# Kernel optimization log

Hardware: AMD Instinct MI355X
Metric: run time of the kernel (lower is better)

The kernel has to match this reference:

```python
import jax, jax.numpy as jnp
import numpy as np

NI = 256        # in_channels
QK = NI // 8    # query/key channels = 32
BS, H, W = 4, 64, 64


def setup_inputs() -> dict:
    key = jax.random.key(0)
    ks = jax.random.split(key, 8)
    x = jax.random.normal(ks[0], (BS, NI, H, W), dtype=jnp.float32)
    # 1x1 conv weights stored as [out_ch, in_ch] (kernel is 1x1)
    wq = jax.random.normal(ks[1], (QK, NI), dtype=jnp.float32) * (1.0 / np.sqrt(NI))
    bq = jnp.zeros((QK,), dtype=jnp.float32)
    wk = jax.random.normal(ks[2], (QK, NI), dtype=jnp.float32) * (1.0 / np.sqrt(NI))
    bk = jnp.zeros((QK,), dtype=jnp.float32)
    wv = jax.random.normal(ks[3], (NI, NI), dtype=jnp.float32) * (1.0 / np.sqrt(NI))
    bv = jnp.zeros((NI,), dtype=jnp.float32)
    # gamma is zero-init in the module; use small random values so the
    # attention branch actually contributes (post-training state).
    gamma = jax.random.normal(ks[4], (1, NI, 1, 1), dtype=jnp.float32) * 0.1
    return {"x": x, "wq": wq, "bq": bq, "wk": wk, "bk": bk,
            "wv": wv, "bv": bv, "gamma": gamma}


def reference(x, wq, bq, wk, bk, wv, bv, gamma):
    bs, c, h, w = x.shape
    n = h * w
    xf = x.reshape(bs, c, n)                       # [bs, c, N]
    # 1x1 convs == per-pixel linear maps over channels
    q = jnp.einsum('oc,bcn->bno', wq, xf) + bq     # [bs, N, qk]
    k = jnp.einsum('oc,bcn->bon', wk, xf) + bk[None, :, None]  # [bs, qk, N]
    v = jnp.einsum('oc,bcn->bon', wv, xf) + bv[None, :, None]  # [bs, c, N]
    attn = jax.nn.softmax(jnp.einsum('bnq,bqm->bnm', q, k), axis=-1)  # [bs, N, N]
    out = jnp.einsum('bcm,bnm->bcn', v, attn)      # value @ attn^T
    out = out.reshape(bs, c, h, w)
    return gamma * out + x
```

## Files before the change

kernel.cpp:

```cpp
#include <hip/hip_runtime.h>
#include <cstdint>
#include <cstddef>

#define NI   256
#define QKC  32
#define BS   4
#define NPIX 4096
#define LOG2E 1.4426950408889634f

typedef __bf16 bf16x8 __attribute__((ext_vector_type(8)));
typedef __bf16 bf16x4 __attribute__((ext_vector_type(4)));
typedef float  f32x16 __attribute__((ext_vector_type(16)));

__device__ inline f32x16 zero16() {
    f32x16 z;
    #pragma unroll
    for (int i = 0; i < 16; ++i) z[i] = 0.f;
    return z;
}

__global__ __launch_bounds__(256) void wconv_pack(
    const float* __restrict__ wq, const float* __restrict__ wk,
    const float* __restrict__ wv, __bf16* __restrict__ wpk)
{
    int f = blockIdx.x * 256 + threadIdx.x;
    int otl = f >> 10, rem = f & 1023;
    int kk = rem >> 6, h = (rem >> 5) & 1, l31 = rem & 31;
    int och = otl * 32 + l31, c0 = kk * 16 + 8 * h;
    const float* src = och < 32 ? wq + och * NI + c0
                     : och < 64 ? wk + (och - 32) * NI + c0
                                : wv + (och - 64) * NI + c0;
    float4 x0 = *(const float4*)src;
    float4 x1 = *(const float4*)(src + 4);
    __align__(16) __bf16 o8[8] = {
        (__bf16)x0.x, (__bf16)x0.y, (__bf16)x0.z, (__bf16)x0.w,
        (__bf16)x1.x, (__bf16)x1.y, (__bf16)x1.z, (__bf16)x1.w};
    *(uint4*)(wpk + (size_t)f * 8) = *(const uint4*)o8;
}

__global__ __launch_bounds__(256) void qkv_mfma(
    const float* __restrict__ x, const __bf16* __restrict__ wpk,
    const float* __restrict__ bq, const float* __restrict__ bk,
    const float* __restrict__ bv,
    __bf16* __restrict__ qpk, __bf16* __restrict__ kpk, __bf16* __restrict__ vpk)
{
    __shared__ __align__(16) __bf16 xT[32][264];
    __shared__ float bls[320];

    const int t = threadIdx.x, w = t >> 6, lane = t & 63;
    const int l31 = lane & 31, h = lane >> 5;
    const int b = blockIdx.y, n0 = blockIdx.x * 32, kt = blockIdx.x;

    for (int i = t; i < 320; i += 256)
        bls[i] = i < 32 ? bq[i] : i < 64 ? bk[i - 32] : bv[i - 64];

    {
        int n4 = (t & 7) * 4, cb = (t >> 3) * 8;
        float4 xv[8];
        #pragma unroll
        for (int j = 0; j < 8; ++j)
            xv[j] = *(const float4*)(x + ((size_t)(b * NI) + cb + j) * NPIX + n0 + n4);
        #pragma unroll
        for (int i = 0; i < 4; ++i) {
            __align__(16) __bf16 r8[8];
            #pragma unroll
            for (int j = 0; j < 8; ++j) r8[j] = (__bf16)((&xv[j].x)[i]);
            *(uint4*)&xT[n4 + i][cb] = *(const uint4*)r8;
        }
    }
    __syncthreads();

    f32x16 acc[3] = {zero16(), zero16(), zero16()};
    #pragma unroll 4
    for (int kk = 0; kk < 16; ++kk) {
        bf16x8 xf = *(const bf16x8*)&xT[l31][kk * 16 + 8 * h];
        #pragma unroll
        for (int jj = 0; jj < 3; ++jj) {
            int otl = w + 4 * jj;
            if (otl < 10) {
                bf16x8 wf = *(const bf16x8*)(wpk + (size_t)((otl * 16 + kk) * 64 + 32 * h + l31) * 8);
                acc[jj] = __builtin_amdgcn_mfma_f32_32x32x16_bf16(wf, xf, acc[jj], 0, 0, 0);
            }
        }
    }
    __syncthreads();

    __bf16 (*vT)[264] = xT;
    #pragma unroll
    for (int jj = 0; jj < 3; ++jj) {
        int otl = w + 4 * jj;
        if (otl >= 2 && otl < 10) {
            #pragma unroll
            for (int qd = 0; qd < 4; ++qd) {
                int c0v = (otl - 2) * 32 + 8 * qd + 4 * h;
                __align__(8) __bf16 q4[4];
                #pragma unroll
                for (int i = 0; i < 4; ++i)
                    q4[i] = (__bf16)(acc[jj][4 * qd + i] + bls[64 + c0v + i]);
                *(uint2*)&vT[l31][c0v] = *(const uint2*)q4;
            }
        }
    }
    #pragma unroll
    for (int jj = 0; jj < 3; ++jj) {
        int otl = w + 4 * jj;
        if (otl == 0) {
            #pragma unroll
            for (int kc = 0; kc < 2; ++kc) {
                __align__(16) __bf16 hi8[8];
                #pragma unroll
                for (int j = 0; j < 8; ++j) {
                    int r = 8 * kc + j;
                    int och = (r & 3) + 8 * (r >> 2) + 4 * h;
                    hi8[j] = (__bf16)((acc[jj][r] + bls[och]) * LOG2E);
                }
                size_t base = ((((size_t)(b * 128 + kt) * 2 + 0) * 2 + kc) * 2 + h) * 32 + l31;
                *(uint4*)(qpk + base * 8) = *(const uint4*)hi8;
            }
        } else if (otl == 1) {
            #pragma unroll
            for (int kc = 0; kc < 2; ++kc) {
                __align__(16) __bf16 k8[8];
                #pragma unroll
                for (int j = 0; j < 8; ++j) {
                    int r = 8 * kc + j;
                    int och = (r & 3) + 8 * (r >> 2) + 4 * h;
                    k8[j] = (__bf16)(acc[jj][r] + bls[32 + och]);
                }
                size_t base = (((size_t)(b * 128 + kt) * 2 + kc) * 2 + h) * 32 + l31;
                *(uint4*)(kpk + base * 8) = *(const uint4*)k8;
            }
        }
    }
    __syncthreads();

    #pragma unroll
    for (int kc = 0; kc < 2; ++kc)
        #pragma unroll
        for (int hh = 0; hh < 2; ++hh) {
            __align__(16) __bf16 f8[8];
            #pragma unroll
            for (int j = 0; j < 8; ++j) f8[j] = vT[16 * kc + 8 * hh + j][t];
            size_t base = (((size_t)(b * 128 + kt) * 2 + kc) * 2 + hh) * 256 + t;
            *(uint4*)(vpk + base * 8) = *(const uint4*)f8;
        }
}

__global__ __launch_bounds__(512, 4) void attn_mfma(
    const __bf16* __restrict__ qpk, const __bf16* __restrict__ kpk,
    const __bf16* __restrict__ vpk,
    __bf16* __restrict__ Opart, float* __restrict__ dpart)
{
    __shared__ __align__(16) __bf16 pt_f[4][2][4][64][8];
    __shared__ float dwave[8][32];

    const int t = threadIdx.x;
    const int b = blockIdx.x & 3, ksp = blockIdx.x >> 2;
    const int n0 = blockIdx.y * 64;
    const int w = t >> 6, lane = t & 63, l31 = lane & 31, h = lane >> 5;
    const int q = w & 3, sr = q & 1, sc = q >> 1, pp = w >> 2;
    const int kt0 = ksp * 64;

    const int qt = 2 * blockIdx.y + sr;
    bf16x8 qf[2];
    #pragma unroll
    for (int kc = 0; kc < 2; ++kc)
        qf[kc] = *(const bf16x8*)(qpk +
            (((((size_t)(b * 128 + qt) * 2 + 0) * 2 + kc) * 2 + h) * 32 + l31) * 8);

    auto kload = [&](int ktile, int kc) {
        return *(const bf16x8*)(kpk +
            ((((size_t)(b * 128 + ktile) * 2 + kc) * 2 + h) * 32 + l31) * 8);
    };
    auto vload = [&](int ktile, int kc) {
        return *(const bf16x8*)(vpk +
            ((((size_t)(b * 128 + ktile) * 2 + kc) * 2 + h) * 256 + 32 * w + l31) * 8);
    };

    f32x16 a0 = zero16(), a1 = zero16();
    float dacc = 0.f;

    auto smma = [&](bf16x8 kh0, bf16x8 kh1) {
        f32x16 s = zero16();
        __builtin_amdgcn_s_setprio(1);
        s = __builtin_amdgcn_mfma_f32_32x32x16_bf16(kh0, qf[0], s, 0, 0, 0);
        s = __builtin_amdgcn_mfma_f32_32x32x16_bf16(kh1, qf[1], s, 0, 0, 0);
        __builtin_amdgcn_s_setprio(0);
        return s;
    };

    auto sfin = [&](const f32x16& s, int buf) {
        unsigned xw[8], xs[8];
        #pragma unroll
        for (int i = 0; i < 8; ++i) {
            float e0 = __builtin_amdgcn_exp2f(s[2 * i]);
            float e1 = __builtin_amdgcn_exp2f(s[2 * i + 1]);
            dacc += e0 + e1;
            __align__(4) __bf16 pr[2] = {(__bf16)e0, (__bf16)e1};
            xw[i] = *(const unsigned*)pr;
        }
        #pragma unroll
        for (int i = 0; i < 8; ++i) xs[i] = __shfl_xor(xw[i], 32);
        const bool hi = (h != 0);
        __align__(16) unsigned f0[4], f1[4];
        f0[0] = hi ? xs[2] : xw[0];  f0[1] = hi ? xs[3] : xw[1];
        f0[2] = hi ? xw[2] : xs[0];  f0[3] = hi ? xw[3] : xs[1];
        f1[0] = hi ? xs[6] : xw[4];  f1[1] = hi ? xs[7] : xw[5];
        f1[2] = hi ? xw[6] : xs[4];  f1[3] = hi ? xw[7] : xs[5];
        *(uint4*)&pt_f[buf][sr][2 * sc + 0][lane][0] = *(const uint4*)f0;
        *(uint4*)&pt_f[buf][sr][2 * sc + 1][lane][0] = *(const uint4*)f1;
    };

    auto pvblock = [&](int mt, const bf16x8 (*vf)[2]) {
        const int buf = mt & 3;
        __builtin_amdgcn_s_setprio(1);
        #pragma unroll
        for (int i = 0; i < 2; ++i)
            #pragma unroll
            for (int kc = 0; kc < 2; ++kc) {
                const int s2 = 2 * i + kc;
                bf16x8 pa0 = *(const bf16x8*)&pt_f[buf][0][s2][lane][0];
                bf16x8 pa1 = *(const bf16x8*)&pt_f[buf][1][s2][lane][0];
                a0 = __builtin_amdgcn_mfma_f32_32x32x16_bf16(pa0, vf[i][kc], a0, 0, 0, 0);
                a1 = __builtin_amdgcn_mfma_f32_32x32x16_bf16(pa1, vf[i][kc], a1, 0, 0, 0);
            }
        __builtin_amdgcn_s_setprio(0);
    };

    bf16x8 kh0 = kload(kt0 + 2 * pp + sc, 0), kh1 = kload(kt0 + 2 * pp + sc, 1);
    {
        f32x16 s = smma(kh0, kh1);
        sfin(s, pp);
    }
    kh0 = kload(kt0 + 2 * (2 + pp) + sc, 0);
    kh1 = kload(kt0 + 2 * (2 + pp) + sc, 1);
    __syncthreads();

    for (int j = 0; j < 16; ++j) {
        f32x16 s;
        if (j < 15) s = smma(kh0, kh1);

        bf16x8 vfa[2][2];
        #pragma unroll
        for (int i = 0; i < 2; ++i)
            #pragma unroll
            for (int kc = 0; kc < 2; ++kc)
                vfa[i][kc] = vload(kt0 + 4 * j + i, kc);

        if (j < 14) {
            const int mtsn = 2 * j + 4 + pp;
            kh0 = kload(kt0 + 2 * mtsn + sc, 0);
            kh1 = kload(kt0 + 2 * mtsn + sc, 1);
        }
        if (j < 15) sfin(s, (2 * j + 2 + pp) & 3);

        bf16x8 vfb[2][2];
        #pragma unroll
        for (int i = 0; i < 2; ++i)
            #pragma unroll
            for (int kc = 0; kc < 2; ++kc)
                vfb[i][kc] = vload(kt0 + 4 * j + 2 + i, kc);

        pvblock(2 * j, vfa);
        pvblock(2 * j + 1, vfb);
        __syncthreads();
    }

    float dtot = dacc + __shfl_xor(dacc, 32);
    if (lane < 32) dwave[w][l31] = dtot;
    __syncthreads();
    if (w < 2 && lane < 32) {
        float dsum = dwave[w][l31] + dwave[w + 2][l31]
                   + dwave[w + 4][l31] + dwave[w + 6][l31];
        dpart[((size_t)(ksp * BS + b)) * NPIX + n0 + 32 * w + l31] = dsum;
    }

    size_t obase = (((size_t)(ksp * BS + b)) * NI + 32 * w + l31) * NPIX + n0;
    #pragma unroll
    for (int rq = 0; rq < 4; ++rq) {
        int nn = 8 * rq + 4 * h;
        __align__(8) __bf16 t0[4], t1[4];
        #pragma unroll
        for (int i = 0; i < 4; ++i) {
            t0[i] = (__bf16)a0[4 * rq + i];
            t1[i] = (__bf16)a1[4 * rq + i];
        }
        *(uint2*)(Opart + obase + nn)      = *(const uint2*)t0;
        *(uint2*)(Opart + obase + 32 + nn) = *(const uint2*)t1;
    }
}

__global__ __launch_bounds__(256) void combine(
    const float* __restrict__ x, const float* __restrict__ gamma,
    const __bf16* __restrict__ Opart, const float* __restrict__ dpart,
    float* __restrict__ out)
{
    int idx = (blockIdx.x * 256 + threadIdx.x) * 4;
    int n = idx & (NPIX - 1);
    int c = (idx >> 12) & (NI - 1);
    int b = idx >> 20;

    size_t o0 = (((size_t)(0 * BS + b)) * NI + c) * NPIX + n;
    size_t o1 = (((size_t)(1 * BS + b)) * NI + c) * NPIX + n;
    bf16x4 p0 = *(const bf16x4*)(Opart + o0);
    bf16x4 p1 = *(const bf16x4*)(Opart + o1);
    float4 da = *(const float4*)(dpart + ((size_t)(0 * BS + b)) * NPIX + n);
    float4 db = *(const float4*)(dpart + ((size_t)(1 * BS + b)) * NPIX + n);
    size_t xb = ((size_t)(b * NI) + c) * NPIX + n;
    float4 xv = *(const float4*)(x + xb);
    float g = gamma[c];

    float4 r;
    r.x = g * (((float)p0[0] + (float)p1[0]) / (da.x + db.x)) + xv.x;
    r.y = g * (((float)p0[1] + (float)p1[1]) / (da.y + db.y)) + xv.y;
    r.z = g * (((float)p0[2] + (float)p1[2]) / (da.z + db.z)) + xv.z;
    r.w = g * (((float)p0[3] + (float)p1[3]) / (da.w + db.w)) + xv.w;
    *(float4*)(out + xb) = r;
}

extern "C" void kernel_launch(void* const* d_in, const int* in_sizes, int n_in,
                              void* d_out, int out_size, void* d_ws, size_t ws_size,
                              hipStream_t stream)
{
    const float* x     = (const float*)d_in[0];
    const float* wq    = (const float*)d_in[1];
    const float* bq    = (const float*)d_in[2];
    const float* wk    = (const float*)d_in[3];
    const float* bk    = (const float*)d_in[4];
    const float* wv    = (const float*)d_in[5];
    const float* bv    = (const float*)d_in[6];
    const float* gamma = (const float*)d_in[7];
    float* out = (float*)d_out;

    const size_t WPK = (size_t)10240 * 8;
    const size_t QPK = (size_t)BS * 128 * 2 * 2 * 2 * 32 * 8;
    const size_t KPK = (size_t)BS * 128 * 2 * 2 * 32 * 8;
    const size_t VPK = (size_t)BS * 128 * 2 * 2 * 256 * 8;
    const size_t OSZ = (size_t)2 * BS * NI * NPIX;
    __bf16* wpk   = (__bf16*)d_ws;
    __bf16* qpk   = wpk + WPK;
    __bf16* kpk   = qpk + QPK;
    __bf16* vpk   = kpk + KPK;
    __bf16* Opart = vpk + VPK;
    float*  dpart = (float*)(Opart + OSZ);

    wconv_pack<<<dim3(40), 256, 0, stream>>>(wq, wk, wv, wpk);
    qkv_mfma<<<dim3(NPIX / 32, BS), 256, 0, stream>>>(x, wpk, bq, bk, bv, qpk, kpk, vpk);
    attn_mfma<<<dim3(8, 64), 512, 0, stream>>>(qpk, kpk, vpk, Opart, dpart);
    combine<<<dim3(BS * NI * NPIX / 1024), 256, 0, stream>>>(x, gamma, Opart, dpart, out);
}
```

Baseline: 154.8 us.

## Fuse split-K combine into attention kernel via last-arriver atomic flags

Removes the separate combine kernel. Each attention block atomically increments a per-(batch, query-tile) flag, and the second of the two key-split blocks to finish merges its own fp32 accumulators (staged through shared memory) with the partner's bf16 partial, normalizes by the summed denominators, and writes gamma*out+x. This skips one kernel launch and avoids having to re-read this block's own partial from global memory. In exchange it adds threadfence and atomic overhead, a larger shared-memory footprint that may reduce occupancy, and a tail of extra work on the finishing blocks. Flags are reset in the weight-pack kernel on each call.

```diff
diff --git a/kernel.cpp b/kernel.cpp
--- a/kernel.cpp
+++ b/kernel.cpp
@@ -21,8 +21,11 @@
 
 __global__ __launch_bounds__(256) void wconv_pack(
     const float* __restrict__ wq, const float* __restrict__ wk,
-    const float* __restrict__ wv, __bf16* __restrict__ wpk)
+    const float* __restrict__ wv, __bf16* __restrict__ wpk,
+    int* __restrict__ flags)
 {
+    if (blockIdx.x == 0) flags[threadIdx.x] = 0;
+
     int f = blockIdx.x * 256 + threadIdx.x;
     int otl = f >> 10, rem = f & 1023;
     int kk = rem >> 6, h = (rem >> 5) & 1, l31 = rem & 31;
@@ -149,10 +152,15 @@
 __global__ __launch_bounds__(512, 4) void attn_mfma(
     const __bf16* __restrict__ qpk, const __bf16* __restrict__ kpk,
     const __bf16* __restrict__ vpk,
-    __bf16* __restrict__ Opart, float* __restrict__ dpart)
+    __bf16* __restrict__ Opart, float* __restrict__ dpart,
+    const float* __restrict__ x, const float* __restrict__ gamma,
+    float* __restrict__ out, int* __restrict__ flags)
 {
-    __shared__ __align__(16) __bf16 pt_f[4][2][4][64][8];
+    __shared__ __align__(16) unsigned char smem[33280];
+    auto pt_f = reinterpret_cast<__bf16 (*)[2][4][64][8]>(smem);
     __shared__ float dwave[8][32];
+    __shared__ float dls[64];
+    __shared__ int who;
 
     const int t = threadIdx.x;
     const int b = blockIdx.x & 3, ksp = blockIdx.x >> 2;
@@ -272,6 +280,7 @@
     if (w < 2 && lane < 32) {
         float dsum = dwave[w][l31] + dwave[w + 2][l31]
                    + dwave[w + 4][l31] + dwave[w + 6][l31];
+        dls[32 * w + l31] = dsum;
         dpart[((size_t)(ksp * BS + b)) * NPIX + n0 + 32 * w + l31] = dsum;
     }
 
@@ -288,34 +297,51 @@
         *(uint2*)(Opart + obase + nn)      = *(const uint2*)t0;
         *(uint2*)(Opart + obase + 32 + nn) = *(const uint2*)t1;
     }
-}
-
-__global__ __launch_bounds__(256) void combine(
-    const float* __restrict__ x, const float* __restrict__ gamma,
-    const __bf16* __restrict__ Opart, const float* __restrict__ dpart,
-    float* __restrict__ out)
-{
-    int idx = (blockIdx.x * 256 + threadIdx.x) * 4;
-    int n = idx & (NPIX - 1);
-    int c = (idx >> 12) & (NI - 1);
-    int b = idx >> 20;
-
-    size_t o0 = (((size_t)(0 * BS + b)) * NI + c) * NPIX + n;
-    size_t o1 = (((size_t)(1 * BS + b)) * NI + c) * NPIX + n;
-    bf16x4 p0 = *(const bf16x4*)(Opart + o0);
-    bf16x4 p1 = *(const bf16x4*)(Opart + o1);
-    float4 da = *(const float4*)(dpart + ((size_t)(0 * BS + b)) * NPIX + n);
-    float4 db = *(const float4*)(dpart + ((size_t)(1 * BS + b)) * NPIX + n);
-    size_t xb = ((size_t)(b * NI) + c) * NPIX + n;
-    float4 xv = *(const float4*)(x + xb);
-    float g = gamma[c];
-
-    float4 r;
-    r.x = g * (((float)p0[0] + (float)p1[0]) / (da.x + db.x)) + xv.x;
-    r.y = g * (((float)p0[1] + (float)p1[1]) / (da.y + db.y)) + xv.y;
-    r.z = g * (((float)p0[2] + (float)p1[2]) / (da.z + db.z)) + xv.z;
-    r.w = g * (((float)p0[3] + (float)p1[3]) / (da.w + db.w)) + xv.w;
-    *(float4*)(out + xb) = r;
+
+    __threadfence();
+    __syncthreads();
+    if (t == 0) who = atomicAdd(&flags[(blockIdx.x & 3) * 64 + blockIdx.y], 1);
+    __syncthreads();
+    if (who == 0) return;
+    __threadfence();
+
+    const int pk = ksp ^ 1;
+    if (t < 64) dls[t] += dpart[((size_t)(pk * BS + b)) * NPIX + n0 + t];
+
+    float* stage = (float*)smem;
+    #pragma unroll 1
+    for (int half = 0; half < 2; ++half) {
+        if ((w >> 2) == half) {
+            int cl = 32 * (w & 3) + l31;
+            #pragma unroll
+            for (int rq = 0; rq < 4; ++rq) {
+                int nn = 8 * rq + 4 * h;
+                #pragma unroll
+                for (int i = 0; i < 4; ++i) {
+                    stage[cl * 65 + nn + i]      = a0[4 * rq + i];
+                    stage[cl * 65 + 32 + nn + i] = a1[4 * rq + i];
+                }
+            }
+        }
+        __syncthreads();
+        int n4 = (t & 15) * 4, cb = t >> 4;
+        #pragma unroll
+        for (int p = 0; p < 4; ++p) {
+            int cl = cb + 32 * p;
+            int c  = 128 * half + cl;
+            bf16x4 pp4 = *(const bf16x4*)(Opart +
+                (((size_t)(pk * BS + b)) * NI + c) * NPIX + n0 + n4);
+            float4 xv = *(const float4*)(x + ((size_t)(b * NI) + c) * NPIX + n0 + n4);
+            float g = gamma[c];
+            float4 r;
+            r.x = g * ((stage[cl * 65 + n4 + 0] + (float)pp4[0]) / dls[n4 + 0]) + xv.x;
+            r.y = g * ((stage[cl * 65 + n4 + 1] + (float)pp4[1]) / dls[n4 + 1]) + xv.y;
+            r.z = g * ((stage[cl * 65 + n4 + 2] + (float)pp4[2]) / dls[n4 + 2]) + xv.z;
+            r.w = g * ((stage[cl * 65 + n4 + 3] + (float)pp4[3]) / dls[n4 + 3]) + xv.w;
+            *(float4*)(out + ((size_t)(b * NI) + c) * NPIX + n0 + n4) = r;
+        }
+        __syncthreads();
+    }
 }
 
 extern "C" void kernel_launch(void* const* d_in, const int* in_sizes, int n_in,
@@ -343,9 +369,10 @@
     __bf16* vpk   = kpk + KPK;
     __bf16* Opart = vpk + VPK;
     float*  dpart = (float*)(Opart + OSZ);
-
-    wconv_pack<<<dim3(40), 256, 0, stream>>>(wq, wk, wv, wpk);
+    int*    flags = (int*)(dpart + (size_t)2 * BS * NPIX);
+
+    wconv_pack<<<dim3(40), 256, 0, stream>>>(wq, wk, wv, wpk, flags);
     qkv_mfma<<<dim3(NPIX / 32, BS), 256, 0, stream>>>(x, wpk, bq, bk, bv, qpk, kpk, vpk);
-    attn_mfma<<<dim3(8, 64), 512, 0, stream>>>(qpk, kpk, vpk, Opart, dpart);
-    combine<<<dim3(BS * NI * NPIX / 1024), 256, 0, stream>>>(x, gamma, Opart, dpart, out);
-}
+    attn_mfma<<<dim3(8, 64), 512, 0, stream>>>(qpk, kpk, vpk, Opart, dpart,
+                                               x, gamma, out, flags);
+}
```

Measured after the change: 351.9 us. +127.2%, slower.

## Fuse split-K combine into attention kernel using 1024-thread blocks with in-LDS reduction

Applied to the files above, without the earlier changes.

The attention kernel drops the two-way key split across blocks. Each block now runs 16 waves, and the two halves of the key range are handled within the block. Partial outputs and softmax denominators are reduced in shared memory, and the gamma-scale plus residual epilogue is applied directly. This removes the separate combine kernel and the bf16 partial-output round trip through global memory. In exchange the grid halves to 256 blocks of 1024 threads and the block uses about 70KB of LDS, which lowers occupancy and parallelism.

```diff
diff --git a/kernel.cpp b/kernel.cpp
--- a/kernel.cpp
+++ b/kernel.cpp
@@ -146,20 +146,22 @@
         }
 }
 
-__global__ __launch_bounds__(512, 4) void attn_mfma(
+__global__ __launch_bounds__(1024, 4) void attn_mfma(
     const __bf16* __restrict__ qpk, const __bf16* __restrict__ kpk,
     const __bf16* __restrict__ vpk,
-    __bf16* __restrict__ Opart, float* __restrict__ dpart)
+    const float* __restrict__ x, const float* __restrict__ gamma,
+    float* __restrict__ out)
 {
-    __shared__ __align__(16) __bf16 pt_f[4][2][4][64][8];
-    __shared__ float dwave[8][32];
+    __shared__ __align__(16) unsigned char smem[69632];
+    auto pt_f = reinterpret_cast<__bf16 (*)[2][4][64][8]>(smem);
+    __shared__ float dwave[16][32];
+    __shared__ float dls[64];
 
     const int t = threadIdx.x;
-    const int b = blockIdx.x & 3, ksp = blockIdx.x >> 2;
+    const int b = blockIdx.x;
     const int n0 = blockIdx.y * 64;
     const int w = t >> 6, lane = t & 63, l31 = lane & 31, h = lane >> 5;
-    const int q = w & 3, sr = q & 1, sc = q >> 1, pp = w >> 2;
-    const int kt0 = ksp * 64;
+    const int q = w & 3, sr = q & 1, sc = q >> 1, g = w >> 2;
 
     const int qt = 2 * blockIdx.y + sr;
     bf16x8 qf[2];
@@ -174,7 +176,8 @@
     };
     auto vload = [&](int ktile, int kc) {
         return *(const bf16x8*)(vpk +
-            ((((size_t)(b * 128 + ktile) * 2 + kc) * 2 + h) * 256 + 32 * w + l31) * 8);
+            ((((size_t)(b * 128 + ktile) * 2 + kc) * 2 + h) * 256
+             + 32 * (w & 7) + l31) * 8);
     };
 
     f32x16 a0 = zero16(), a1 = zero16();
@@ -212,7 +215,7 @@
     };
 
     auto pvblock = [&](int mt, const bf16x8 (*vf)[2]) {
-        const int buf = mt & 3;
+        const int buf = mt & 7;
         __builtin_amdgcn_s_setprio(1);
         #pragma unroll
         for (int i = 0; i < 2; ++i)
@@ -227,95 +230,99 @@
         __builtin_amdgcn_s_setprio(0);
     };
 
-    bf16x8 kh0 = kload(kt0 + 2 * pp + sc, 0), kh1 = kload(kt0 + 2 * pp + sc, 1);
+    bf16x8 kh0 = kload(2 * g + sc, 0), kh1 = kload(2 * g + sc, 1);
     {
         f32x16 s = smma(kh0, kh1);
-        sfin(s, pp);
-    }
-    kh0 = kload(kt0 + 2 * (2 + pp) + sc, 0);
-    kh1 = kload(kt0 + 2 * (2 + pp) + sc, 1);
+        sfin(s, g);
+    }
+    kh0 = kload(2 * (4 + g) + sc, 0);
+    kh1 = kload(2 * (4 + g) + sc, 1);
     __syncthreads();
 
     for (int j = 0; j < 16; ++j) {
         f32x16 s;
         if (j < 15) s = smma(kh0, kh1);
 
+        const int tb = 4 * j + (w >> 3);
         bf16x8 vfa[2][2];
         #pragma unroll
         for (int i = 0; i < 2; ++i)
             #pragma unroll
             for (int kc = 0; kc < 2; ++kc)
-                vfa[i][kc] = vload(kt0 + 4 * j + i, kc);
+                vfa[i][kc] = vload(2 * tb + i, kc);
 
         if (j < 14) {
-            const int mtsn = 2 * j + 4 + pp;
-            kh0 = kload(kt0 + 2 * mtsn + sc, 0);
-            kh1 = kload(kt0 + 2 * mtsn + sc, 1);
-        }
-        if (j < 15) sfin(s, (2 * j + 2 + pp) & 3);
+            const int nt = 4 * j + 8 + g;
+            kh0 = kload(2 * nt + sc, 0);
+            kh1 = kload(2 * nt + sc, 1);
+        }
+        if (j < 15) sfin(s, (4 * j + 4 + g) & 7);
 
         bf16x8 vfb[2][2];
         #pragma unroll
         for (int i = 0; i < 2; ++i)
             #pragma unroll
             for (int kc = 0; kc < 2; ++kc)
-                vfb[i][kc] = vload(kt0 + 4 * j + 2 + i, kc);
-
-        pvblock(2 * j, vfa);
-        pvblock(2 * j + 1, vfb);
+                vfb[i][kc] = vload(2 * (tb + 2) + i, kc);
+
+        pvblock(tb, vfa);
+        pvblock(tb + 2, vfb);
         __syncthreads();
     }
 
     float dtot = dacc + __shfl_xor(dacc, 32);
     if (lane < 32) dwave[w][l31] = dtot;
     __syncthreads();
-    if (w < 2 && lane < 32) {
-        float dsum = dwave[w][l31] + dwave[w + 2][l31]
-                   + dwave[w + 4][l31] + dwave[w + 6][l31];
-        dpart[((size_t)(ksp * BS + b)) * NPIX + n0 + 32 * w + l31] = dsum;
-    }
-
-    size_t obase = (((size_t)(ksp * BS + b)) * NI + 32 * w + l31) * NPIX + n0;
-    #pragma unroll
-    for (int rq = 0; rq < 4; ++rq) {
-        int nn = 8 * rq + 4 * h;
-        __align__(8) __bf16 t0[4], t1[4];
-        #pragma unroll
-        for (int i = 0; i < 4; ++i) {
-            t0[i] = (__bf16)a0[4 * rq + i];
-            t1[i] = (__bf16)a1[4 * rq + i];
-        }
-        *(uint2*)(Opart + obase + nn)      = *(const uint2*)t0;
-        *(uint2*)(Opart + obase + 32 + nn) = *(const uint2*)t1;
-    }
-}
-
-__global__ __launch_bounds__(256) void combine(
-    const float* __restrict__ x, const float* __restrict__ gamma,
-    const __bf16* __restrict__ Opart, const float* __restrict__ dpart,
-    float* __restrict__ out)
-{
-    int idx = (blockIdx.x * 256 + threadIdx.x) * 4;
-    int n = idx & (NPIX - 1);
-    int c = (idx >> 12) & (NI - 1);
-    int b = idx >> 20;
-
-    size_t o0 = (((size_t)(0 * BS + b)) * NI + c) * NPIX + n;
-    size_t o1 = (((size_t)(1 * BS + b)) * NI + c) * NPIX + n;
-    bf16x4 p0 = *(const bf16x4*)(Opart + o0);
-    bf16x4 p1 = *(const bf16x4*)(Opart + o1);
-    float4 da = *(const float4*)(dpart + ((size_t)(0 * BS + b)) * NPIX + n);
-    float4 db = *(const float4*)(dpart + ((size_t)(1 * BS + b)) * NPIX + n);
-    size_t xb = ((size_t)(b * NI) + c) * NPIX + n;
-    float4 xv = *(const float4*)(x + xb);
-    float g = gamma[c];
-
-    float4 r;
-    r.x = g * (((float)p0[0] + (float)p1[0]) / (da.x + db.x)) + xv.x;
-    r.y = g * (((float)p0[1] + (float)p1[1]) / (da.y + db.y)) + xv.y;
-    r.z = g * (((float)p0[2] + (float)p1[2]) / (da.z + db.z)) + xv.z;
-    r.w = g * (((float)p0[3] + (float)p1[3]) / (da.w + db.w)) + xv.w;
-    *(float4*)(out + xb) = r;
+
+    float* stage = (float*)smem;
+    if (t < 64) {
+        float ds = 0.f;
+        #pragma unroll
+        for (int k = 0; k < 8; ++k) ds += dwave[2 * k + (t >> 5)][t & 31];
+        dls[t] = ds;
+    }
+    if (w < 8) {
+        float* sc_ = stage + (32 * (w & 7) + l31) * 68;
+        #pragma unroll
+        for (int rq = 0; rq < 4; ++rq) {
+            int nn = 8 * rq + 4 * h;
+            #pragma unroll
+            for (int i = 0; i < 4; ++i) {
+                sc_[nn + i]      = a0[4 * rq + i];
+                sc_[32 + nn + i] = a1[4 * rq + i];
+            }
+        }
+    }
+    __syncthreads();
+    if (w >= 8) {
+        float* sc_ = stage + (32 * (w & 7) + l31) * 68;
+        #pragma unroll
+        for (int rq = 0; rq < 4; ++rq) {
+            int nn = 8 * rq + 4 * h;
+            #pragma unroll
+            for (int i = 0; i < 4; ++i) {
+                sc_[nn + i]      += a0[4 * rq + i];
+                sc_[32 + nn + i] += a1[4 * rq + i];
+            }
+        }
+    }
+    __syncthreads();
+
+    const int n4 = (t & 15) * 4, c0 = t >> 4;
+    #pragma unroll
+    for (int p = 0; p < 4; ++p) {
+        const int c = c0 + 64 * p;
+        const float gm = gamma[c];
+        size_t xb = ((size_t)(b * NI) + c) * NPIX + n0 + n4;
+        float4 xv = *(const float4*)(x + xb);
+        const float* sc_ = stage + c * 68 + n4;
+        float4 r;
+        r.x = gm * (sc_[0] / dls[n4 + 0]) + xv.x;
+        r.y = gm * (sc_[1] / dls[n4 + 1]) + xv.y;
+        r.z = gm * (sc_[2] / dls[n4 + 2]) + xv.z;
+        r.w = gm * (sc_[3] / dls[n4 + 3]) + xv.w;
+        *(float4*)(out + xb) = r;
+    }
 }
 
 extern "C" void kernel_launch(void* const* d_in, const int* in_sizes, int n_in,
@@ -335,17 +342,12 @@
     const size_t WPK = (size_t)10240 * 8;
     const size_t QPK = (size_t)BS * 128 * 2 * 2 * 2 * 32 * 8;
     const size_t KPK = (size_t)BS * 128 * 2 * 2 * 32 * 8;
-    const size_t VPK = (size_t)BS * 128 * 2 * 2 * 256 * 8;
-    const size_t OSZ = (size_t)2 * BS * NI * NPIX;
     __bf16* wpk   = (__bf16*)d_ws;
     __bf16* qpk   = wpk + WPK;
     __bf16* kpk   = qpk + QPK;
     __bf16* vpk   = kpk + KPK;
-    __bf16* Opart = vpk + VPK;
-    float*  dpart = (float*)(Opart + OSZ);
 
     wconv_pack<<<dim3(40), 256, 0, stream>>>(wq, wk, wv, wpk);
     qkv_mfma<<<dim3(NPIX / 32, BS), 256, 0, stream>>>(x, wpk, bq, bk, bv, qpk, kpk, vpk);
-    attn_mfma<<<dim3(8, 64), 512, 0, stream>>>(qpk, kpk, vpk, Opart, dpart);
-    combine<<<dim3(BS * NI * NPIX / 1024), 256, 0, stream>>>(x, gamma, Opart, dpart, out);
-}
+    attn_mfma<<<dim3(4, 64), 1024, 0, stream>>>(qpk, kpk, vpk, x, gamma, out);
+}
```

Result: faster. 146.3 us (-5.5%).
